# Kernel optimization log

Hardware: AMD Instinct MI355X
Metric: run time of the kernel (lower is better)

Reference implementation:

```python
import jax, jax.numpy as jnp
import numpy as np

N = 50000
E = 800000
D_IN, D_HID, D_OUT = 128, 128, 64


def setup_inputs() -> dict:
    key = jax.random.key(0)
    ks = jax.random.split(key, 8)
    x = jax.random.normal(ks[0], (N, D_IN), dtype=jnp.float32)
    edge_index = jax.random.randint(ks[1], (2, E), 0, N, dtype=jnp.int64)
    # SAGEConv params: lin_l (neighbors, with bias), lin_r (root, no bias)
    s1 = 1.0 / np.sqrt(D_IN)
    s2 = 1.0 / np.sqrt(D_HID)
    W1_l = jax.random.uniform(ks[2], (D_IN, D_HID), jnp.float32, -s1, s1)
    b1 = jnp.zeros((D_HID,), jnp.float32)
    W1_r = jax.random.uniform(ks[3], (D_IN, D_HID), jnp.float32, -s1, s1)
    W2_l = jax.random.uniform(ks[4], (D_HID, D_OUT), jnp.float32, -s2, s2)
    b2 = jnp.zeros((D_OUT,), jnp.float32)
    W2_r = jax.random.uniform(ks[5], (D_HID, D_OUT), jnp.float32, -s2, s2)
    return {"x": x, "edge_index": edge_index, "W1_l": W1_l, "b1": b1,
            "W1_r": W1_r, "W2_l": W2_l, "b2": b2, "W2_r": W2_r}


def _sage_conv(x, src, dst, Wl, b, Wr, num_nodes):
    # mean aggregation over incoming edges (src -> dst)
    msgs = x[src]                                              # [E, d]
    agg = jax.ops.segment_sum(msgs, dst, num_segments=num_nodes)
    cnt = jax.ops.segment_sum(jnp.ones((src.shape[0],), x.dtype), dst,
                              num_segments=num_nodes)
    mean = agg / jnp.clip(cnt, 1.0)[:, None]                   # [N, d]
    return mean @ Wl + b + x @ Wr


def reference(x, edge_index, W1_l, b1, W1_r, W2_l, b2, W2_r):
    src, dst = edge_index[0], edge_index[1]
    n = x.shape[0]
    h = jax.nn.relu(_sage_conv(x, src, dst, W1_l, b1, W1_r, n))
    # dropout p=0.5 is identity in eval mode (training=False)
    return _sage_conv(h, src, dst, W2_l, b2, W2_r, n)
```

## Files before the change

kernel.cpp:

```cpp
#include <hip/hip_runtime.h>
#include <hip/hip_bf16.h>

typedef __hip_bfloat16 bf16;
typedef __attribute__((ext_vector_type(8))) short short8;
typedef __attribute__((ext_vector_type(4))) float floatx4;
typedef __attribute__((ext_vector_type(2))) float floatx2;
typedef unsigned short u16;
typedef unsigned char u8;

#define NNODES 50000
#define NEDGES 800000
#define D_IN  128
#define D_HID 128
#define D_OUT 64
#define NBLK  ((NNODES + 255) / 256)

__device__ __forceinline__ float bfbits2f(unsigned int u) {
    return __uint_as_float(u << 16);
}
__device__ __forceinline__ float b2f(bf16 v) { return __bfloat162float(v); }
__device__ __forceinline__ unsigned short f2bfbits(float f) {
    bf16 b = __float2bfloat16(f);
    return *(unsigned short*)&b;
}
__device__ __forceinline__ u8 f2fp8(float f) {
    return (u8)(__builtin_amdgcn_cvt_pk_fp8_f32(f, 0.f, 0, false) & 0xFF);
}
__device__ __forceinline__ float fp8tof(unsigned int u) {
    floatx2 v = __builtin_amdgcn_cvt_pk_f32_fp8(u, false);
    return v.x;
}
__device__ __forceinline__ float ld(const void* p, long long idx, int isf32) {
    if (isf32) return ((const float*)p)[idx];
    return b2f(((const bf16*)p)[idx]);
}
__device__ __forceinline__ short8 a_frag_from(const void* xp, long long elem_off, int isf32) {
    if (!isf32) return *(const short8*)((const bf16*)xp + elem_off);
    const float* f = (const float*)xp + elem_off;
    short8 r;
    #pragma unroll
    for (int j = 0; j < 8; j++) r[j] = (short)f2bfbits(f[j]);
    return r;
}

__global__ void k_setup(int* __restrict__ cnt, int n,
                        const unsigned int* __restrict__ ei_words,
                        const unsigned int* __restrict__ w_words,
                        int* __restrict__ flags,
                        const void* __restrict__ x,
                        const void* __restrict__ W1l, const void* __restrict__ W1r,
                        const void* __restrict__ W2l, const void* __restrict__ W2r,
                        bf16* __restrict__ p1l, bf16* __restrict__ p1r,
                        bf16* __restrict__ p2l, bf16* __restrict__ p2r,
                        unsigned int* __restrict__ x8) {
    int b = blockIdx.x;
    if (b < 128) {
        if (b == 0) {
            __shared__ int cnt_zero, cnt_bf;
            if (threadIdx.x == 0) { cnt_zero = 0; cnt_bf = 0; }
            __syncthreads();
            int t = threadIdx.x;
            unsigned int we = ei_words[2 * t + 1];
            if (we == 0u) atomicAdd(&cnt_zero, 1);
            unsigned int ww = w_words[t];
            unsigned int lowexp = (ww >> 7) & 0xFFu;
            if (lowexp >= 0x60u && lowexp <= 0x7Bu) atomicAdd(&cnt_bf, 1);
            __syncthreads();
            if (threadIdx.x == 0) {
                flags[0] = (cnt_zero >= 240) ? 1 : 0;
                flags[1] = (cnt_bf >= 192) ? 0 : 1;
            }
        }
        int i = b * blockDim.x + threadIdx.x;
        int stride = 128 * blockDim.x;
        for (; i < n; i += stride) cnt[i] = 0;
        return;
    }
    __shared__ int cnt_bf2;
    if (threadIdx.x == 0) cnt_bf2 = 0;
    __syncthreads();
    {
        unsigned int ww = w_words[threadIdx.x];
        unsigned int lowexp = (ww >> 7) & 0xFFu;
        if (lowexp >= 0x60u && lowexp <= 0x7Bu) atomicAdd(&cnt_bf2, 1);
    }
    __syncthreads();
    int isf32 = (cnt_bf2 >= 192) ? 0 : 1;
    if (b < 152) {
        int t = (b - 128) * 256 + threadIdx.x;
        if (t >= 6144) return;
        const void* Wm; bf16* dst; int NT; int base;
        if (t < 2048)      { Wm = W1l; dst = p1l; NT = 8; base = t; }
        else if (t < 4096) { Wm = W1r; dst = p1r; NT = 8; base = t - 2048; }
        else if (t < 5120) { Wm = W2l; dst = p2l; NT = 4; base = t - 4096; }
        else               { Wm = W2r; dst = p2r; NT = 4; base = t - 5120; }
        int lane = base & 63;
        int kt = (base >> 6) & 3;
        int nt = base >> 8;
        int Nmat = NT * 16;
        int krow = kt * 32 + ((lane >> 4) * 8);
        int col = nt * 16 + (lane & 15);
        #pragma unroll
        for (int j = 0; j < 8; j++) {
            float v = ld(Wm, (long long)(krow + j) * Nmat + col, isf32);
            dst[(((nt * 4 + kt) * 64 + lane) * 8) + j] = __float2bfloat16(v);
        }
        return;
    }
    const long long NU32 = (long long)NNODES * D_IN / 4;
    long long i = (long long)(b - 152) * 256 + threadIdx.x;
    long long stride = (long long)(gridDim.x - 152) * 256;
    for (; i < NU32; i += stride) {
        long long e0 = i * 4;
        float f0 = ld(x, e0 + 0, isf32);
        float f1 = ld(x, e0 + 1, isf32);
        float f2 = ld(x, e0 + 2, isf32);
        float f3 = ld(x, e0 + 3, isf32);
        unsigned int w0 = __builtin_amdgcn_cvt_pk_fp8_f32(f0, f1, 0, false);
        w0 = __builtin_amdgcn_cvt_pk_fp8_f32(f2, f3, w0, true);
        x8[i] = w0;
    }
}

__global__ void k_edges(const int* __restrict__ ei, const int* __restrict__ flags,
                        u16* __restrict__ src16, unsigned int* __restrict__ drpack,
                        int* __restrict__ cnt) {
    int e = blockIdx.x * blockDim.x + threadIdx.x;
    if (e >= NEDGES) return;
    int s, d;
    if (flags[0]) { s = ei[2 * e]; d = ei[2 * (NEDGES + e)]; }
    else          { s = ei[e];     d = ei[NEDGES + e]; }
    src16[e] = (u16)s;
    int rank = atomicAdd(&cnt[d], 1);
    drpack[e] = ((unsigned int)rank << 16) | (unsigned int)d;
}

__global__ void k_scan_a(const int* __restrict__ cnt, int* __restrict__ excl,
                         int* __restrict__ bsum) {
    __shared__ int s[256];
    int t = threadIdx.x;
    int i = blockIdx.x * 256 + t;
    int v = (i < NNODES) ? cnt[i] : 0;
    s[t] = v;
    __syncthreads();
    for (int off = 1; off < 256; off <<= 1) {
        int u = (t >= off) ? s[t - off] : 0;
        __syncthreads();
        s[t] += u;
        __syncthreads();
    }
    if (i < NNODES) excl[i] = s[t] - v;
    if (t == 255) bsum[blockIdx.x] = s[255];
}

__global__ void k_scan_bc(const int* __restrict__ excl, const int* __restrict__ bsum,
                          int* __restrict__ row_start) {
    __shared__ int s[256];
    __shared__ int bo;
    int t = threadIdx.x;
    int v = (t < NBLK) ? bsum[t] : 0;
    s[t] = v;
    __syncthreads();
    for (int off = 1; off < 256; off <<= 1) {
        int u = (t >= off) ? s[t - off] : 0;
        __syncthreads();
        s[t] += u;
        __syncthreads();
    }
    if (t == 0) bo = s[blockIdx.x] - bsum[blockIdx.x];
    __syncthreads();
    int i = blockIdx.x * 256 + t;
    if (i < NNODES) row_start[i] = bo + excl[i];
    if (i == 0) row_start[NNODES] = NEDGES;
}

__global__ void k_scatter(const u16* __restrict__ src16,
                          const unsigned int* __restrict__ drpack,
                          const int* __restrict__ row_start,
                          u16* __restrict__ csr16) {
    int e = blockIdx.x * blockDim.x + threadIdx.x;
    if (e >= NEDGES) return;
    unsigned int dp = drpack[e];
    int d = (int)(dp & 0xFFFFu);
    int r = (int)(dp >> 16);
    csr16[row_start[d] + r] = src16[e];
}

__global__ __launch_bounds__(256) void k_l1fused(
        const int* __restrict__ row_start, const u16* __restrict__ csr16,
        const void* __restrict__ x, const u16* __restrict__ x8u,
        const int* __restrict__ flags,
        const bf16* __restrict__ p1l, const bf16* __restrict__ p1r,
        const bf16* __restrict__ p2l, const bf16* __restrict__ p2r,
        const void* __restrict__ b1, const void* __restrict__ b2v,
        u8* __restrict__ h28, float* __restrict__ hrf) {
    __shared__ bf16 ms[16][136];
    __shared__ bf16 hs[16][136];
    __shared__ u8 h2s8[16][72];
    __shared__ float hrs[16][68];
    int t = threadIdx.x;
    int w = t >> 6;
    int l = t & 63;
    int nb = blockIdx.x * 16;
    int isf32 = flags[1];

    for (int i = 0; i < 4; i++) {
        int ln = w * 4 + i;
        int node = nb + ln;
        int s0 = row_start[node], s1 = row_start[node + 1];
        float a0 = 0.f, a1 = 0.f;
        for (int base = s0; base < s1; base += 64) {
            int cnt2 = min(64, s1 - base);
            int my = (l < cnt2) ? (int)csr16[base + l] : 0;
            int j = 0;
            for (; j + 7 < cnt2; j += 8) {
                int i0 = __shfl(my, j + 0), i1 = __shfl(my, j + 1);
                int i2 = __shfl(my, j + 2), i3 = __shfl(my, j + 3);
                int i4 = __shfl(my, j + 4), i5 = __shfl(my, j + 5);
                int i6 = __shfl(my, j + 6), i7 = __shfl(my, j + 7);
                unsigned int u0 = x8u[(size_t)i0 * 64 + l];
                unsigned int u1 = x8u[(size_t)i1 * 64 + l];
                unsigned int u2 = x8u[(size_t)i2 * 64 + l];
                unsigned int u3 = x8u[(size_t)i3 * 64 + l];
                unsigned int u4 = x8u[(size_t)i4 * 64 + l];
                unsigned int u5 = x8u[(size_t)i5 * 64 + l];
                unsigned int u6 = x8u[(size_t)i6 * 64 + l];
                unsigned int u7 = x8u[(size_t)i7 * 64 + l];
                floatx2 v0 = __builtin_amdgcn_cvt_pk_f32_fp8(u0, false);
                floatx2 v1 = __builtin_amdgcn_cvt_pk_f32_fp8(u1, false);
                floatx2 v2 = __builtin_amdgcn_cvt_pk_f32_fp8(u2, false);
                floatx2 v3 = __builtin_amdgcn_cvt_pk_f32_fp8(u3, false);
                floatx2 v4 = __builtin_amdgcn_cvt_pk_f32_fp8(u4, false);
                floatx2 v5 = __builtin_amdgcn_cvt_pk_f32_fp8(u5, false);
                floatx2 v6 = __builtin_amdgcn_cvt_pk_f32_fp8(u6, false);
                floatx2 v7 = __builtin_amdgcn_cvt_pk_f32_fp8(u7, false);
                a0 += v0.x + v1.x + v2.x + v3.x + v4.x + v5.x + v6.x + v7.x;
                a1 += v0.y + v1.y + v2.y + v3.y + v4.y + v5.y + v6.y + v7.y;
            }
            for (; j < cnt2; j++) {
                int si = __shfl(my, j);
                unsigned int u = x8u[(size_t)si * 64 + l];
                floatx2 v = __builtin_amdgcn_cvt_pk_f32_fp8(u, false);
                a0 += v.x; a1 += v.y;
            }
        }
        float inv = 1.0f / fmaxf((float)(s1 - s0), 1.0f);
        unsigned int pk = ((unsigned int)f2bfbits(a1 * inv) << 16) | f2bfbits(a0 * inv);
        *(unsigned int*)((bf16*)&ms[ln][0] + l * 2) = pk;
    }
    __syncthreads();

    int m = l & 15;
    int quad = l >> 4;
    floatx4 acc0 = {0.f, 0.f, 0.f, 0.f};
    floatx4 acc1 = {0.f, 0.f, 0.f, 0.f};
    short8 am[4], ax[4];
    long long rowoff = (long long)(nb + m) * D_IN;
    #pragma unroll
    for (int kt = 0; kt < 4; kt++) {
        am[kt] = *(const short8*)&ms[m][kt * 32 + quad * 8];
        ax[kt] = a_frag_from(x, rowoff + kt * 32 + quad * 8, isf32);
    }
    int nt0 = w * 2, nt1 = w * 2 + 1;
    #pragma unroll
    for (int kt = 0; kt < 4; kt++) {
        short8 bl0 = *(const short8*)(p1l + (((nt0 * 4 + kt) * 64 + l) * 8));
        short8 br0 = *(const short8*)(p1r + (((nt0 * 4 + kt) * 64 + l) * 8));
        acc0 = __builtin_amdgcn_mfma_f32_16x16x32_bf16(am[kt], bl0, acc0, 0, 0, 0);
        acc0 = __builtin_amdgcn_mfma_f32_16x16x32_bf16(ax[kt], br0, acc0, 0, 0, 0);
        short8 bl1 = *(const short8*)(p1l + (((nt1 * 4 + kt) * 64 + l) * 8));
        short8 br1 = *(const short8*)(p1r + (((nt1 * 4 + kt) * 64 + l) * 8));
        acc1 = __builtin_amdgcn_mfma_f32_16x16x32_bf16(am[kt], bl1, acc1, 0, 0, 0);
        acc1 = __builtin_amdgcn_mfma_f32_16x16x32_bf16(ax[kt], br1, acc1, 0, 0, 0);
    }
    int c0 = nt0 * 16 + m;
    int c1 = nt1 * 16 + m;
    float bias0 = ld(b1, c0, isf32);
    float bias1 = ld(b1, c1, isf32);
    #pragma unroll
    for (int r = 0; r < 4; r++) {
        int row = quad * 4 + r;
        hs[row][c0] = __float2bfloat16(fmaxf(acc0[r] + bias0, 0.f));
        hs[row][c1] = __float2bfloat16(fmaxf(acc1[r] + bias1, 0.f));
    }
    __syncthreads();
    floatx4 acc2 = {0.f, 0.f, 0.f, 0.f};
    floatx4 acc3 = {0.f, 0.f, 0.f, 0.f};
    #pragma unroll
    for (int kt = 0; kt < 4; kt++) {
        short8 ah = *(const short8*)&hs[m][kt * 32 + quad * 8];
        short8 bw = *(const short8*)(p2l + (((w * 4 + kt) * 64 + l) * 8));
        short8 bz = *(const short8*)(p2r + (((w * 4 + kt) * 64 + l) * 8));
        acc2 = __builtin_amdgcn_mfma_f32_16x16x32_bf16(ah, bw, acc2, 0, 0, 0);
        acc3 = __builtin_amdgcn_mfma_f32_16x16x32_bf16(ah, bz, acc3, 0, 0, 0);
    }
    int c2 = w * 16 + m;
    float bias2 = ld(b2v, c2, isf32);
    #pragma unroll
    for (int r = 0; r < 4; r++) {
        h2s8[quad * 4 + r][c2] = f2fp8(acc2[r]);
        hrs[quad * 4 + r][c2] = acc3[r] + bias2;
    }
    __syncthreads();
    if (t < 128) {
        int node = t >> 3, col0 = (t & 7) * 8;
        uint2 v = *(const uint2*)&h2s8[node][col0];
        *(uint2*)(h28 + (long long)(nb + node) * D_OUT + col0) = v;
    }
    {
        int node = t >> 4, col0 = (t & 15) * 4;
        float4 v = *(const float4*)&hrs[node][col0];
        *(float4*)(hrf + (long long)(nb + node) * D_OUT + col0) = v;
    }
}

__global__ void k_agg2g(const int* __restrict__ row_start, const u16* __restrict__ csr16,
                        const u8* __restrict__ h28, const float* __restrict__ hrf,
                        const int* __restrict__ flags, void* __restrict__ out) {
    int t = threadIdx.x;
    int lane = t & 63;
    int node = blockIdx.x * 4 + (t >> 6);
    int s0 = row_start[node], s1 = row_start[node + 1];
    float a = 0.f;
    for (int base = s0; base < s1; base += 64) {
        int cnt2 = min(64, s1 - base);
        int my = (lane < cnt2) ? (int)csr16[base + lane] : 0;
        int j = 0;
        for (; j + 7 < cnt2; j += 8) {
            int i0 = __shfl(my, j + 0), i1 = __shfl(my, j + 1);
            int i2 = __shfl(my, j + 2), i3 = __shfl(my, j + 3);
            int i4 = __shfl(my, j + 4), i5 = __shfl(my, j + 5);
            int i6 = __shfl(my, j + 6), i7 = __shfl(my, j + 7);
            unsigned int u0 = h28[(size_t)i0 * D_OUT + lane];
            unsigned int u1 = h28[(size_t)i1 * D_OUT + lane];
            unsigned int u2 = h28[(size_t)i2 * D_OUT + lane];
            unsigned int u3 = h28[(size_t)i3 * D_OUT + lane];
            unsigned int u4 = h28[(size_t)i4 * D_OUT + lane];
            unsigned int u5 = h28[(size_t)i5 * D_OUT + lane];
            unsigned int u6 = h28[(size_t)i6 * D_OUT + lane];
            unsigned int u7 = h28[(size_t)i7 * D_OUT + lane];
            a += fp8tof(u0) + fp8tof(u1) + fp8tof(u2) + fp8tof(u3)
               + fp8tof(u4) + fp8tof(u5) + fp8tof(u6) + fp8tof(u7);
        }
        for (; j < cnt2; j++) {
            int si = __shfl(my, j);
            a += fp8tof((unsigned int)h28[(size_t)si * D_OUT + lane]);
        }
    }
    float inv = 1.0f / fmaxf((float)(s1 - s0), 1.0f);
    float acc = a * inv + hrf[(size_t)node * D_OUT + lane];
    if (flags[1]) ((float*)out)[(size_t)node * D_OUT + lane] = acc;
    else          ((bf16*)out)[(size_t)node * D_OUT + lane] = __float2bfloat16(acc);
}

extern "C" void kernel_launch(void* const* d_in, const int* in_sizes, int n_in,
                              void* d_out, int out_size, void* d_ws, size_t ws_size,
                              hipStream_t stream) {
    const void* x   = d_in[0];
    const int*  ei  = (const int*)d_in[1];
    const void* W1l = d_in[2];
    const void* b1  = d_in[3];
    const void* W1r = d_in[4];
    const void* W2l = d_in[5];
    const void* b2v = d_in[6];
    const void* W2r = d_in[7];

    const int N = NNODES;
    const int E = NEDGES;

    int*          flags     = (int*)d_ws;
    u16*          src16     = (u16*)(flags + 4);
    unsigned int* drpack    = (unsigned int*)(src16 + E);
    int*          cnt       = (int*)(drpack + E);
    int*          excl      = cnt + N;
    int*          bsum      = excl + N;
    int*          row_start = bsum + 256;
    u16*          csr16     = (u16*)(row_start + (N + 16));
    bf16*         p1l       = (bf16*)(csr16 + E);
    bf16*         p1r       = p1l + 16384;
    bf16*         p2l       = p1r + 16384;
    bf16*         p2r       = p2l + 8192;
    unsigned int* x8        = (unsigned int*)(p2r + 8192);
    u8*           h28       = (u8*)(x8 + (size_t)N * D_IN / 4);
    float*        hrf       = (float*)(h28 + (size_t)N * D_OUT);

    k_setup<<<152 + 1024, 256, 0, stream>>>(cnt, N, (const unsigned int*)ei,
                                            (const unsigned int*)W1l, flags, x,
                                            W1l, W1r, W2l, W2r,
                                            p1l, p1r, p2l, p2r, x8);
    k_edges<<<(E + 255) / 256, 256, 0, stream>>>(ei, flags, src16, drpack, cnt);
    k_scan_a<<<NBLK, 256, 0, stream>>>(cnt, excl, bsum);
    k_scan_bc<<<NBLK, 256, 0, stream>>>(excl, bsum, row_start);
    k_scatter<<<(E + 255) / 256, 256, 0, stream>>>(src16, drpack, row_start, csr16);
    k_l1fused<<<N / 16, 256, 0, stream>>>(row_start, csr16, x, (const u16*)x8, flags,
                                          p1l, p1r, p2l, p2r, b1, b2v, h28, hrf);
    k_agg2g<<<N / 4, 256, 0, stream>>>(row_start, csr16, h28, hrf, flags, d_out);
}
```

Baseline: 219.5 us.

## Widen gather loads to 32-bit fp8 words and split edges across wave halves

Layer-1 aggregation now loads 4 fp8 features per lane as a dword, so half a wave covers a 128-wide row and the two halves process different edges before a cross-half shuffle reduction. Layer-2 aggregation does the same with 16 lanes per row and four edge groups, and writes outputs as vector stores. The x-to-fp8 conversion uses float4/ushort4 vector loads, and row_start is read once per wave and shuffled. This is meant to cut the number of memory instructions and sub-dword loads in the gather loops, at the cost of more complex tail handling and extra shuffle reductions.

New measurement: 214.1 us. 1.03x faster.

```diff
diff --git a/kernel.cpp b/kernel.cpp
--- a/kernel.cpp
+++ b/kernel.cpp
@@ -25,10 +25,6 @@
 }
 __device__ __forceinline__ u8 f2fp8(float f) {
     return (u8)(__builtin_amdgcn_cvt_pk_fp8_f32(f, 0.f, 0, false) & 0xFF);
-}
-__device__ __forceinline__ float fp8tof(unsigned int u) {
-    floatx2 v = __builtin_amdgcn_cvt_pk_f32_fp8(u, false);
-    return v.x;
 }
 __device__ __forceinline__ float ld(const void* p, long long idx, int isf32) {
     if (isf32) return ((const float*)p)[idx];
@@ -110,15 +106,24 @@
     const long long NU32 = (long long)NNODES * D_IN / 4;
     long long i = (long long)(b - 152) * 256 + threadIdx.x;
     long long stride = (long long)(gridDim.x - 152) * 256;
-    for (; i < NU32; i += stride) {
-        long long e0 = i * 4;
-        float f0 = ld(x, e0 + 0, isf32);
-        float f1 = ld(x, e0 + 1, isf32);
-        float f2 = ld(x, e0 + 2, isf32);
-        float f3 = ld(x, e0 + 3, isf32);
-        unsigned int w0 = __builtin_amdgcn_cvt_pk_fp8_f32(f0, f1, 0, false);
-        w0 = __builtin_amdgcn_cvt_pk_fp8_f32(f2, f3, w0, true);
-        x8[i] = w0;
+    if (isf32) {
+        const float4* xf = (const float4*)x;
+        for (; i < NU32; i += stride) {
+            float4 f = xf[i];
+            unsigned int w0 = __builtin_amdgcn_cvt_pk_fp8_f32(f.x, f.y, 0, false);
+            w0 = __builtin_amdgcn_cvt_pk_fp8_f32(f.z, f.w, w0, true);
+            x8[i] = w0;
+        }
+    } else {
+        const ushort4* xb = (const ushort4*)x;
+        for (; i < NU32; i += stride) {
+            ushort4 s = xb[i];
+            float f0 = bfbits2f(s.x), f1 = bfbits2f(s.y);
+            float f2 = bfbits2f(s.z), f3 = bfbits2f(s.w);
+            unsigned int w0 = __builtin_amdgcn_cvt_pk_fp8_f32(f0, f1, 0, false);
+            w0 = __builtin_amdgcn_cvt_pk_fp8_f32(f2, f3, w0, true);
+            x8[i] = w0;
+        }
     }
 }
 
@@ -188,7 +193,7 @@
 
 __global__ __launch_bounds__(256) void k_l1fused(
         const int* __restrict__ row_start, const u16* __restrict__ csr16,
-        const void* __restrict__ x, const u16* __restrict__ x8u,
+        const void* __restrict__ x, const unsigned int* __restrict__ x8w,
         const int* __restrict__ flags,
         const bf16* __restrict__ p1l, const bf16* __restrict__ p1r,
         const bf16* __restrict__ p2l, const bf16* __restrict__ p2r,
@@ -203,50 +208,101 @@
     int l = t & 63;
     int nb = blockIdx.x * 16;
     int isf32 = flags[1];
+    int h = l >> 5;
+    int c = l & 31;
+
+    int rsv = row_start[nb + w * 4 + min(l, 4)];
 
     for (int i = 0; i < 4; i++) {
         int ln = w * 4 + i;
-        int node = nb + ln;
-        int s0 = row_start[node], s1 = row_start[node + 1];
-        float a0 = 0.f, a1 = 0.f;
+        int s0 = __shfl(rsv, i), s1 = __shfl(rsv, i + 1);
+        float a0 = 0.f, a1 = 0.f, a2 = 0.f, a3 = 0.f;
         for (int base = s0; base < s1; base += 64) {
             int cnt2 = min(64, s1 - base);
             int my = (l < cnt2) ? (int)csr16[base + l] : 0;
             int j = 0;
+            for (; j + 15 < cnt2; j += 16) {
+                int jb = j + h * 8;
+                int i0 = __shfl(my, jb + 0), i1 = __shfl(my, jb + 1);
+                int i2 = __shfl(my, jb + 2), i3 = __shfl(my, jb + 3);
+                int i4 = __shfl(my, jb + 4), i5 = __shfl(my, jb + 5);
+                int i6 = __shfl(my, jb + 6), i7 = __shfl(my, jb + 7);
+                unsigned int u0 = x8w[(size_t)i0 * 32 + c];
+                unsigned int u1 = x8w[(size_t)i1 * 32 + c];
+                unsigned int u2 = x8w[(size_t)i2 * 32 + c];
+                unsigned int u3 = x8w[(size_t)i3 * 32 + c];
+                unsigned int u4 = x8w[(size_t)i4 * 32 + c];
+                unsigned int u5 = x8w[(size_t)i5 * 32 + c];
+                unsigned int u6 = x8w[(size_t)i6 * 32 + c];
+                unsigned int u7 = x8w[(size_t)i7 * 32 + c];
+                floatx2 l0 = __builtin_amdgcn_cvt_pk_f32_fp8(u0, false);
+                floatx2 h0 = __builtin_amdgcn_cvt_pk_f32_fp8(u0, true);
+                floatx2 l1 = __builtin_amdgcn_cvt_pk_f32_fp8(u1, false);
+                floatx2 h1 = __builtin_amdgcn_cvt_pk_f32_fp8(u1, true);
+                floatx2 l2 = __builtin_amdgcn_cvt_pk_f32_fp8(u2, false);
+                floatx2 h2 = __builtin_amdgcn_cvt_pk_f32_fp8(u2, true);
+                floatx2 l3 = __builtin_amdgcn_cvt_pk_f32_fp8(u3, false);
+                floatx2 h3 = __builtin_amdgcn_cvt_pk_f32_fp8(u3, true);
+                floatx2 l4 = __builtin_amdgcn_cvt_pk_f32_fp8(u4, false);
+                floatx2 h4 = __builtin_amdgcn_cvt_pk_f32_fp8(u4, true);
+                floatx2 l5 = __builtin_amdgcn_cvt_pk_f32_fp8(u5, false);
+                floatx2 h5 = __builtin_amdgcn_cvt_pk_f32_fp8(u5, true);
+                floatx2 l6 = __builtin_amdgcn_cvt_pk_f32_fp8(u6, false);
+                floatx2 h6 = __builtin_amdgcn_cvt_pk_f32_fp8(u6, true);
+                floatx2 l7 = __builtin_amdgcn_cvt_pk_f32_fp8(u7, false);
+                floatx2 h7 = __builtin_amdgcn_cvt_pk_f32_fp8(u7, true);
+                a0 += l0.x + l1.x + l2.x + l3.x + l4.x + l5.x + l6.x + l7.x;
+                a1 += l0.y + l1.y + l2.y + l3.y + l4.y + l5.y + l6.y + l7.y;
+                a2 += h0.x + h1.x + h2.x + h3.x + h4.x + h5.x + h6.x + h7.x;
+                a3 += h0.y + h1.y + h2.y + h3.y + h4.y + h5.y + h6.y + h7.y;
+            }
             for (; j + 7 < cnt2; j += 8) {
-                int i0 = __shfl(my, j + 0), i1 = __shfl(my, j + 1);
-                int i2 = __shfl(my, j + 2), i3 = __shfl(my, j + 3);
-                int i4 = __shfl(my, j + 4), i5 = __shfl(my, j + 5);
-                int i6 = __shfl(my, j + 6), i7 = __shfl(my, j + 7);
-                unsigned int u0 = x8u[(size_t)i0 * 64 + l];
-                unsigned int u1 = x8u[(size_t)i1 * 64 + l];
-                unsigned int u2 = x8u[(size_t)i2 * 64 + l];
-                unsigned int u3 = x8u[(size_t)i3 * 64 + l];
-                unsigned int u4 = x8u[(size_t)i4 * 64 + l];
-                unsigned int u5 = x8u[(size_t)i5 * 64 + l];
-                unsigned int u6 = x8u[(size_t)i6 * 64 + l];
-                unsigned int u7 = x8u[(size_t)i7 * 64 + l];
-                floatx2 v0 = __builtin_amdgcn_cvt_pk_f32_fp8(u0, false);
-                floatx2 v1 = __builtin_amdgcn_cvt_pk_f32_fp8(u1, false);
-                floatx2 v2 = __builtin_amdgcn_cvt_pk_f32_fp8(u2, false);
-                floatx2 v3 = __builtin_amdgcn_cvt_pk_f32_fp8(u3, false);
-                floatx2 v4 = __builtin_amdgcn_cvt_pk_f32_fp8(u4, false);
-                floatx2 v5 = __builtin_amdgcn_cvt_pk_f32_fp8(u5, false);
-                floatx2 v6 = __builtin_amdgcn_cvt_pk_f32_fp8(u6, false);
-                floatx2 v7 = __builtin_amdgcn_cvt_pk_f32_fp8(u7, false);
-                a0 += v0.x + v1.x + v2.x + v3.x + v4.x + v5.x + v6.x + v7.x;
-                a1 += v0.y + v1.y + v2.y + v3.y + v4.y + v5.y + v6.y + v7.y;
+                int jb = j + h * 4;
+                int i0 = __shfl(my, jb + 0), i1 = __shfl(my, jb + 1);
+                int i2 = __shfl(my, jb + 2), i3 = __shfl(my, jb + 3);
+                unsigned int u0 = x8w[(size_t)i0 * 32 + c];
+                unsigned int u1 = x8w[(size_t)i1 * 32 + c];
+                unsigned int u2 = x8w[(size_t)i2 * 32 + c];
+                unsigned int u3 = x8w[(size_t)i3 * 32 + c];
+                floatx2 l0 = __builtin_amdgcn_cvt_pk_f32_fp8(u0, false);
+                floatx2 h0 = __builtin_amdgcn_cvt_pk_f32_fp8(u0, true);
+                floatx2 l1 = __builtin_amdgcn_cvt_pk_f32_fp8(u1, false);
+                floatx2 h1 = __builtin_amdgcn_cvt_pk_f32_fp8(u1, true);
+                floatx2 l2 = __builtin_amdgcn_cvt_pk_f32_fp8(u2, false);
+                floatx2 h2 = __builtin_amdgcn_cvt_pk_f32_fp8(u2, true);
+                floatx2 l3 = __builtin_amdgcn_cvt_pk_f32_fp8(u3, false);
+                floatx2 h3 = __builtin_amdgcn_cvt_pk_f32_fp8(u3, true);
+                a0 += l0.x + l1.x + l2.x + l3.x;
+                a1 += l0.y + l1.y + l2.y + l3.y;
+                a2 += h0.x + h1.x + h2.x + h3.x;
+                a3 += h0.y + h1.y + h2.y + h3.y;
             }
-            for (; j < cnt2; j++) {
-                int si = __shfl(my, j);
-                unsigned int u = x8u[(size_t)si * 64 + l];
-                floatx2 v = __builtin_amdgcn_cvt_pk_f32_fp8(u, false);
-                a0 += v.x; a1 += v.y;
+            for (; j + 1 < cnt2; j += 2) {
+                int i0 = __shfl(my, j + h);
+                unsigned int u0 = x8w[(size_t)i0 * 32 + c];
+                floatx2 l0 = __builtin_amdgcn_cvt_pk_f32_fp8(u0, false);
+                floatx2 h0 = __builtin_amdgcn_cvt_pk_f32_fp8(u0, true);
+                a0 += l0.x; a1 += l0.y; a2 += h0.x; a3 += h0.y;
             }
-        }
-        float inv = 1.0f / fmaxf((float)(s1 - s0), 1.0f);
-        unsigned int pk = ((unsigned int)f2bfbits(a1 * inv) << 16) | f2bfbits(a0 * inv);
-        *(unsigned int*)((bf16*)&ms[ln][0] + l * 2) = pk;
+            if (j < cnt2) {
+                int i0 = __shfl(my, j);
+                unsigned int u0 = x8w[(size_t)i0 * 32 + c];
+                floatx2 l0 = __builtin_amdgcn_cvt_pk_f32_fp8(u0, false);
+                floatx2 h0 = __builtin_amdgcn_cvt_pk_f32_fp8(u0, true);
+                if (h == 0) { a0 += l0.x; a1 += l0.y; a2 += h0.x; a3 += h0.y; }
+            }
+        }
+        a0 += __shfl_xor(a0, 32);
+        a1 += __shfl_xor(a1, 32);
+        a2 += __shfl_xor(a2, 32);
+        a3 += __shfl_xor(a3, 32);
+        if (l < 32) {
+            float inv = 1.0f / fmaxf((float)(s1 - s0), 1.0f);
+            uint2 pk;
+            pk.x = ((unsigned int)f2bfbits(a1 * inv) << 16) | f2bfbits(a0 * inv);
+            pk.y = ((unsigned int)f2bfbits(a3 * inv) << 16) | f2bfbits(a2 * inv);
+            *(uint2*)((bf16*)&ms[ln][0] + (c << 2)) = pk;
+        }
     }
     __syncthreads();
 
@@ -320,37 +376,81 @@
     int t = threadIdx.x;
     int lane = t & 63;
     int node = blockIdx.x * 4 + (t >> 6);
+    int g = lane >> 4;
+    int c = lane & 15;
+    const unsigned int* h32 = (const unsigned int*)h28;
     int s0 = row_start[node], s1 = row_start[node + 1];
-    float a = 0.f;
+    float a0 = 0.f, a1 = 0.f, a2 = 0.f, a3 = 0.f;
     for (int base = s0; base < s1; base += 64) {
         int cnt2 = min(64, s1 - base);
         int my = (lane < cnt2) ? (int)csr16[base + lane] : 0;
         int j = 0;
+        for (; j + 15 < cnt2; j += 16) {
+            int i0 = __shfl(my, j + g);
+            int i1 = __shfl(my, j + 4 + g);
+            int i2 = __shfl(my, j + 8 + g);
+            int i3 = __shfl(my, j + 12 + g);
+            unsigned int u0 = h32[(size_t)i0 * 16 + c];
+            unsigned int u1 = h32[(size_t)i1 * 16 + c];
+            unsigned int u2 = h32[(size_t)i2 * 16 + c];
+            unsigned int u3 = h32[(size_t)i3 * 16 + c];
+            floatx2 l0 = __builtin_amdgcn_cvt_pk_f32_fp8(u0, false);
+            floatx2 h0 = __builtin_amdgcn_cvt_pk_f32_fp8(u0, true);
+            floatx2 l1 = __builtin_amdgcn_cvt_pk_f32_fp8(u1, false);
+            floatx2 h1 = __builtin_amdgcn_cvt_pk_f32_fp8(u1, true);
+            floatx2 l2 = __builtin_amdgcn_cvt_pk_f32_fp8(u2, false);
+            floatx2 h2 = __builtin_amdgcn_cvt_pk_f32_fp8(u2, true);
+            floatx2 l3 = __builtin_amdgcn_cvt_pk_f32_fp8(u3, false);
+            floatx2 h3 = __builtin_amdgcn_cvt_pk_f32_fp8(u3, true);
+            a0 += l0.x + l1.x + l2.x + l3.x;
+            a1 += l0.y + l1.y + l2.y + l3.y;
+            a2 += h0.x + h1.x + h2.x + h3.x;
+            a3 += h0.y + h1.y + h2.y + h3.y;
+        }
         for (; j + 7 < cnt2; j += 8) {
-            int i0 = __shfl(my, j + 0), i1 = __shfl(my, j + 1);
-            int i2 = __shfl(my, j + 2), i3 = __shfl(my, j + 3);
-            int i4 = __shfl(my, j + 4), i5 = __shfl(my, j + 5);
-            int i6 = __shfl(my, j + 6), i7 = __shfl(my, j + 7);
-            unsigned int u0 = h28[(size_t)i0 * D_OUT + lane];
-            unsigned int u1 = h28[(size_t)i1 * D_OUT + lane];
-            unsigned int u2 = h28[(size_t)i2 * D_OUT + lane];
-            unsigned int u3 = h28[(size_t)i3 * D_OUT + lane];
-            unsigned int u4 = h28[(size_t)i4 * D_OUT + lane];
-            unsigned int u5 = h28[(size_t)i5 * D_OUT + lane];
-            unsigned int u6 = h28[(size_t)i6 * D_OUT + lane];
-            unsigned int u7 = h28[(size_t)i7 * D_OUT + lane];
-            a += fp8tof(u0) + fp8tof(u1) + fp8tof(u2) + fp8tof(u3)
-               + fp8tof(u4) + fp8tof(u5) + fp8tof(u6) + fp8tof(u7);
-        }
-        for (; j < cnt2; j++) {
-            int si = __shfl(my, j);
-            a += fp8tof((unsigned int)h28[(size_t)si * D_OUT + lane]);
-        }
-    }
-    float inv = 1.0f / fmaxf((float)(s1 - s0), 1.0f);
-    float acc = a * inv + hrf[(size_t)node * D_OUT + lane];
-    if (flags[1]) ((float*)out)[(size_t)node * D_OUT + lane] = acc;
-    else          ((bf16*)out)[(size_t)node * D_OUT + lane] = __float2bfloat16(acc);
+            int i0 = __shfl(my, j + g);
+            int i1 = __shfl(my, j + 4 + g);
+            unsigned int u0 = h32[(size_t)i0 * 16 + c];
+            unsigned int u1 = h32[(size_t)i1 * 16 + c];
+            floatx2 l0 = __builtin_amdgcn_cvt_pk_f32_fp8(u0, false);
+            floatx2 h0 = __builtin_amdgcn_cvt_pk_f32_fp8(u0, true);
+            floatx2 l1 = __builtin_amdgcn_cvt_pk_f32_fp8(u1, false);
+            floatx2 h1 = __builtin_amdgcn_cvt_pk_f32_fp8(u1, true);
+            a0 += l0.x + l1.x; a1 += l0.y + l1.y;
+            a2 += h0.x + h1.x; a3 += h0.y + h1.y;
+        }
+        for (; j < cnt2; j += 4) {
+            int jj = j + g;
+            float mk = (jj < cnt2) ? 1.0f : 0.0f;
+            int i0 = __shfl(my, jj & 63);
+            unsigned int u0 = h32[(size_t)i0 * 16 + c];
+            floatx2 l0 = __builtin_amdgcn_cvt_pk_f32_fp8(u0, false);
+            floatx2 h0 = __builtin_amdgcn_cvt_pk_f32_fp8(u0, true);
+            a0 += mk * l0.x; a1 += mk * l0.y;
+            a2 += mk * h0.x; a3 += mk * h0.y;
+        }
+    }
+    a0 += __shfl_xor(a0, 32); a0 += __shfl_xor(a0, 16);
+    a1 += __shfl_xor(a1, 32); a1 += __shfl_xor(a1, 16);
+    a2 += __shfl_xor(a2, 32); a2 += __shfl_xor(a2, 16);
+    a3 += __shfl_xor(a3, 32); a3 += __shfl_xor(a3, 16);
+    if (lane < 16) {
+        float inv = 1.0f / fmaxf((float)(s1 - s0), 1.0f);
+        const float4 hr = *(const float4*)&hrf[(size_t)node * D_OUT + (c << 2)];
+        float o0 = a0 * inv + hr.x;
+        float o1 = a1 * inv + hr.y;
+        float o2 = a2 * inv + hr.z;
+        float o3 = a3 * inv + hr.w;
+        if (flags[1]) {
+            float4 v = {o0, o1, o2, o3};
+            *(float4*)((float*)out + (size_t)node * D_OUT + (c << 2)) = v;
+        } else {
+            uint2 v;
+            v.x = ((unsigned int)f2bfbits(o1) << 16) | f2bfbits(o0);
+            v.y = ((unsigned int)f2bfbits(o3) << 16) | f2bfbits(o2);
+            *(uint2*)((bf16*)out + (size_t)node * D_OUT + (c << 2)) = v;
+        }
+    }
 }
 
 extern "C" void kernel_launch(void* const* d_in, const int* in_sizes, int n_in,
@@ -392,7 +492,7 @@
     k_scan_a<<<NBLK, 256, 0, stream>>>(cnt, excl, bsum);
     k_scan_bc<<<NBLK, 256, 0, stream>>>(excl, bsum, row_start);
     k_scatter<<<(E + 255) / 256, 256, 0, stream>>>(src16, drpack, row_start, csr16);
-    k_l1fused<<<N / 16, 256, 0, stream>>>(row_start, csr16, x, (const u16*)x8, flags,
+    k_l1fused<<<N / 16, 256, 0, stream>>>(row_start, csr16, x, x8, flags,
                                           p1l, p1r, p2l, p2r, b1, b2v, h28, hrf);
     k_agg2g<<<N / 4, 256, 0, stream>>>(row_start, csr16, h28, hrf, flags, d_out);
 }
```
